# Kernel optimization log

Hardware: AMD Instinct MI355X
Metric: run time of the kernel (lower is better)

## Reference

```python
import jax, jax.numpy as jnp
import numpy as np

BATCH, INPUTDIM, OUTDIM, GRIDSIZE = 4096, 256, 256, 64


def setup_inputs() -> dict:
    key = jax.random.key(0)
    k1, k2 = jax.random.split(key)
    x = jax.random.normal(k1, (BATCH, INPUTDIM), dtype=jnp.float32)
    # xavier_uniform over (2, outdim, inputdim, gridsize): fan_in = inputdim*gridsize, fan_out = outdim*gridsize
    fan_in = INPUTDIM * GRIDSIZE
    fan_out = OUTDIM * GRIDSIZE
    limit = float(np.sqrt(6.0 / (fan_in + fan_out)))
    fouriercoeffs = jax.random.uniform(
        k2, (2, OUTDIM, INPUTDIM, GRIDSIZE), dtype=jnp.float32,
        minval=-limit, maxval=limit)
    bias = jnp.zeros((1, OUTDIM), dtype=jnp.float32)
    return {"x": x, "fouriercoeffs": fouriercoeffs, "bias": bias}


def reference(x, fouriercoeffs, bias):
    # x: [B, inputdim]; fouriercoeffs: [2, outdim, inputdim, gridsize]; bias: [1, outdim]
    # gridsize_param is clamp/round'ed to an int in torch -> static = initial_gridsize here.
    G = fouriercoeffs.shape[-1]
    k = jnp.arange(1, G + 1, dtype=x.dtype)        # [G] frequencies 1..G
    xk = x[:, :, None] * k                          # [B, inputdim, G]
    c = jnp.cos(xk)                                 # [B, inputdim, G]
    s = jnp.sin(xk)                                 # [B, inputdim, G]
    # Fused contraction over (inputdim, gridsize) -- avoids the naive
    # [B, outdim, inputdim, gridsize] broadcast tensor of the torch code.
    y = (jnp.einsum('big,oig->bo', c, fouriercoeffs[0])
         + jnp.einsum('big,oig->bo', s, fouriercoeffs[1])
         + bias)                                    # [B, outdim]
    return y
```

## Files before the change

kernel.cpp:

```cpp
#include <hip/hip_runtime.h>
#include <hip/hip_bf16.h>


typedef __attribute__((ext_vector_type(8))) short short8;
typedef __attribute__((ext_vector_type(4))) float f32x4;

#define SPLITK 8
#define ICHUNK (256 / SPLITK)

#define INV2PI 0.15915494309189535f

#if __has_builtin(__builtin_amdgcn_cvt_pk_bf16_f32)
typedef __attribute__((ext_vector_type(2))) __bf16 bf16x2_t;
__device__ __forceinline__ unsigned pkbf16(float a, float b) {
    bf16x2_t v = __builtin_amdgcn_cvt_pk_bf16_f32(a, b);
    return __builtin_bit_cast(unsigned, v);
}
#else
__device__ __forceinline__ unsigned pkbf16(float a, float b) {
    unsigned ua = __builtin_bit_cast(unsigned, a) + 0x8000u;
    unsigned ub = __builtin_bit_cast(unsigned, b) + 0x8000u;
    return __builtin_amdgcn_perm(ub, ua, 0x07060302u);
}
#endif

__device__ __forceinline__ void dbl2(float c, float s, float& co, float& so) {
    float t = c + c;
    co = __builtin_fmaf(t, c, -1.f);
    so = t * s;
}
__device__ __forceinline__ void rot2(float c, float s, float cr, float sr,
                                     float& co, float& so) {
    float t = s * sr;
    co = __builtin_fmaf(c, cr, -t);
    float u = s * cr;
    so = __builtin_fmaf(c, sr, u);
}

__device__ __forceinline__ short8 chain8(float m1, float fm1, float f0) {
    unsigned r[4];
    float vp = fm1, v = f0;
    #pragma unroll
    for (int h = 0; h < 4; ++h) {
        float v1 = __builtin_fmaf(m1, v, -vp);
        r[h] = pkbf16(v, v1);
        float v2 = __builtin_fmaf(m1, v1, -v);
        vp = v1; v = v2;
    }
    uint4 u; u.x = r[0]; u.y = r[1]; u.z = r[2]; u.w = r[3];
    return __builtin_bit_cast(short8, u);
}

__device__ __forceinline__ void async_load16(const void* g, void* l) {
    __builtin_amdgcn_global_load_lds(
        (const __attribute__((address_space(1))) unsigned int*)g,
        (__attribute__((address_space(3))) unsigned int*)l,
        16, 0, 0);
}

__global__ __launch_bounds__(256) void prep_kernel(
    const float* __restrict__ fc, const float* __restrict__ bias,
    unsigned short* __restrict__ ws2, float* __restrict__ out)
{
    const unsigned bid = blockIdx.x;
    const unsigned t = threadIdx.x;
    if (bid < 4096) {
        unsigned flat = bid * 256 + t;
        unsigned bx = flat >> 11, gi = flat & 2047;
        unsigned i = bx >> 1, y = bx & 1;
        unsigned sog = gi >> 6, ll = gi & 63;
        unsigned s = sog >> 3, og = sog & 7;
        unsigned op = og * 16 + (ll & 15);
        unsigned k = s * 32 + ((ll >> 4) * 8);
        unsigned tt = k >> 6, g0 = k & 63;
        const float4* src = (const float4*)(fc +
            ((((size_t)tt * 256 + y * 128 + op) * 256 + i) * 64 + g0));
        float4 a = src[0], b = src[1];
        uint4 v;
        v.x = pkbf16(a.x, a.y); v.y = pkbf16(a.z, a.w);
        v.z = pkbf16(b.x, b.y); v.w = pkbf16(b.z, b.w);
        ((uint4*)ws2)[flat] = v;
    } else {
        int tid = (bid - 4096) * 256 + t;
        float4 b4 = ((const float4*)bias)[tid & 63];
        ((float4*)out)[tid] = b4;
    }
}

template <bool USE_WS>
__global__ __launch_bounds__(256, 2) void fkan_gemm(
    const float* __restrict__ x, const float* __restrict__ fc,
    const unsigned short* __restrict__ bws, float* __restrict__ out)
{
    __shared__ uint4 Bimg[2][2048];
    __shared__ float xs[ICHUNK][128];

    const int t  = threadIdx.x;
    const int l  = t & 63;
    const int w  = t >> 6;
    const int wr = w >> 1, wc = w & 1;
    const int q  = l >> 4;
    const int m  = l & 15;

    const int bid = blockIdx.x;
    const int z   = bid & 7;
    const int by  = (bid >> 3) & 1;
    const int bx  = bid >> 4;
    const int rowBase = bx * 128;
    const int iBase   = z * ICHUNK;

    f32x4 acc[4][4];
    #pragma unroll
    for (int a = 0; a < 4; ++a)
        #pragma unroll
        for (int b = 0; b < 4; ++b) acc[a][b] = (f32x4)0.0f;

    auto stageB = [&](int p, int i) {
        if (USE_WS) {
            const unsigned short* base = bws + ((size_t)(i * 2 + by) * 2048) * 8;
            #pragma unroll
            for (int cc = 0; cc < 8; ++cc) {
                int c = cc * 4 + w;
                async_load16(base + (size_t)(c * 64 + l) * 8, (void*)(&Bimg[p][c * 64]));
            }
        } else {
            #pragma unroll
            for (int gg = 0; gg < 8; ++gg) {
                int gi  = gg * 256 + t;
                int sog = gi >> 6, ll = gi & 63;
                int s = sog >> 3, ogb = sog & 7;
                int o = ogb * 16 + (ll & 15);
                int k = s * 32 + (ll >> 4) * 8;
                int tt = k >> 6, g = k & 63;
                const float4* p4 = (const float4*)(fc +
                    ((((size_t)tt * 256 + by * 128 + o) * 256 + i) * 64 + g));
                float4 a = p4[0], b = p4[1];
                uint4 v;
                v.x = pkbf16(a.x, a.y); v.y = pkbf16(a.z, a.w);
                v.z = pkbf16(b.x, b.y); v.w = pkbf16(b.z, b.w);
                Bimg[p][gi] = v;
            }
        }
    };

    stageB(0, iBase);
    {
        int r = t >> 1, c0 = (t & 1) * 16;
        const float4* px = (const float4*)(x + (size_t)(rowBase + r) * 256 + iBase + c0);
        float4 v0 = px[0], v1 = px[1], v2 = px[2], v3 = px[3];
        float tmp[16] = { v0.x, v0.y, v0.z, v0.w, v1.x, v1.y, v1.z, v1.w,
                          v2.x, v2.y, v2.z, v2.w, v3.x, v3.y, v3.z, v3.w };
        #pragma unroll
        for (int j = 0; j < 16; ++j) xs[c0 + j][r] = tmp[j];
    }
    __syncthreads();

    #pragma unroll 1
    for (int ii = 0; ii < ICHUNK; ++ii) {
        const int p = ii & 1;

        if (ii + 1 < ICHUNK) stageB(p ^ 1, iBase + ii + 1);

        short8 bF[4][4];
        #pragma unroll
        for (int s = 0; s < 4; ++s)
            #pragma unroll
            for (int cf = 0; cf < 4; ++cf)
                bF[s][cf] = __builtin_bit_cast(short8,
                    Bimg[p][(s * 8 + wc * 4 + cf) * 64 + l]);

        short8 aF[4][4];
        #pragma unroll
        for (int rf = 0; rf < 4; ++rf) {
            float xv = xs[ii][wr * 64 + rf * 16 + m];
            float rev = xv * INV2PI;
            float s1 = __builtin_amdgcn_sinf(rev);
            float c1 = __builtin_amdgcn_cosf(rev);
            const float m1 = c1 + c1;
            float c2, s2, c4, s4, c8, s8, c16, s16, c32, s32;
            dbl2(c1, s1, c2, s2);
            dbl2(c2, s2, c4, s4);
            dbl2(c4, s4, c8, s8);
            dbl2(c8, s8, c16, s16);
            dbl2(c16, s16, c32, s32);
            float c24, s24;
            rot2(c16, s16, c8, s8, c24, s24);
            float cq = (q == 0) ? 1.f : (q == 1) ? c8 : (q == 2) ? c16 : c24;
            float sq = (q == 0) ? 0.f : (q == 1) ? s8 : (q == 2) ? s16 : s24;
            float cq1, sq1, cB, sB, cB1, sB1;
            rot2(cq, sq, c1, s1, cq1, sq1);
            rot2(cq, sq, c32, s32, cB, sB);
            rot2(cB, sB, c1, s1, cB1, sB1);
            aF[rf][0] = chain8(m1, cq, cq1);
            aF[rf][1] = chain8(m1, cB, cB1);
            aF[rf][2] = chain8(m1, sq, sq1);
            aF[rf][3] = chain8(m1, sB, sB1);
        }

        #pragma unroll
        for (int s = 0; s < 4; ++s)
            #pragma unroll
            for (int rf = 0; rf < 4; ++rf)
                #pragma unroll
                for (int cf = 0; cf < 4; ++cf)
                    acc[rf][cf] = __builtin_amdgcn_mfma_f32_16x16x32_bf16(
                        aF[rf][s], bF[s][cf], acc[rf][cf], 0, 0, 0);

        __syncthreads();
    }

    const int r0 = rowBase + wr * 64 + (l >> 4) * 4;
    const int c0 = by * 128 + wc * 64 + m;
    #pragma unroll
    for (int rf = 0; rf < 4; ++rf)
        #pragma unroll
        for (int cf = 0; cf < 4; ++cf)
            #pragma unroll
            for (int e = 0; e < 4; ++e)
                atomicAdd(out + (size_t)(r0 + rf * 16 + e) * 256 + (c0 + cf * 16),
                          acc[rf][cf][e]);
}

extern "C" void kernel_launch(void* const* d_in, const int* in_sizes, int n_in,
                              void* d_out, int out_size, void* d_ws, size_t ws_size,
                              hipStream_t stream) {
    const float* x    = (const float*)d_in[0];
    const float* fc   = (const float*)d_in[1];
    const float* bias = (const float*)d_in[2];
    float* out = (float*)d_out;
    unsigned short* bws = (unsigned short*)d_ws;

    const size_t wsNeed = (size_t)512 * 2048 * 16;
    hipLaunchKernelGGL(prep_kernel, dim3(5120), dim3(256), 0, stream,
                       fc, bias, bws, out);
    if (ws_size >= wsNeed) {
        hipLaunchKernelGGL((fkan_gemm<true>), dim3(512), dim3(256), 0, stream,
                           x, fc, bws, out);
    } else {
        hipLaunchKernelGGL((fkan_gemm<false>), dim3(512), dim3(256), 0, stream,
                           x, fc, bws, out);
    }
}
```

Before: 177.1 us.

## Replace split-K atomic adds with partial buffers and a separate reduce kernel

Each split-K block now writes its partial tile to a per-slice workspace buffer with plain stores. A new reduce kernel then sums the eight slices and adds the bias. This removes contended global float atomics on the output, but adds a third launch and about 32 MB of extra partial-buffer writes and reads. The old atomic path is kept as a fallback when the workspace is too small.

```diff
diff --git a/kernel.cpp b/kernel.cpp
--- a/kernel.cpp
+++ b/kernel.cpp
@@ -60,9 +60,9 @@
 
 __global__ __launch_bounds__(256) void prep_kernel(
     const float* __restrict__ fc, const float* __restrict__ bias,
-    unsigned short* __restrict__ ws2, float* __restrict__ out)
+    unsigned short* __restrict__ ws2, float* __restrict__ out, int base)
 {
-    const unsigned bid = blockIdx.x;
+    const unsigned bid = blockIdx.x + base;
     const unsigned t = threadIdx.x;
     if (bid < 4096) {
         unsigned flat = bid * 256 + t;
@@ -87,10 +87,26 @@
     }
 }
 
-template <bool USE_WS>
+__global__ __launch_bounds__(256) void reduce_kernel(
+    const float* __restrict__ pws, const float* __restrict__ bias,
+    float* __restrict__ out)
+{
+    int idx4 = blockIdx.x * 256 + threadIdx.x;
+    const float4* p4 = (const float4*)pws;
+    float4 r = ((const float4*)bias)[idx4 & 63];
+    #pragma unroll
+    for (int z = 0; z < SPLITK; ++z) {
+        float4 v = p4[(size_t)z * 262144 + idx4];
+        r.x += v.x; r.y += v.y; r.z += v.z; r.w += v.w;
+    }
+    ((float4*)out)[idx4] = r;
+}
+
+template <bool USE_WS, bool PARTIAL>
 __global__ __launch_bounds__(256, 2) void fkan_gemm(
     const float* __restrict__ x, const float* __restrict__ fc,
-    const unsigned short* __restrict__ bws, float* __restrict__ out)
+    const unsigned short* __restrict__ bws, float* __restrict__ out,
+    float* __restrict__ pws)
 {
     __shared__ uint4 Bimg[2][2048];
     __shared__ float xs[ICHUNK][128];
@@ -211,14 +227,26 @@
 
     const int r0 = rowBase + wr * 64 + (l >> 4) * 4;
     const int c0 = by * 128 + wc * 64 + m;
-    #pragma unroll
-    for (int rf = 0; rf < 4; ++rf)
-        #pragma unroll
-        for (int cf = 0; cf < 4; ++cf)
-            #pragma unroll
-            for (int e = 0; e < 4; ++e)
-                atomicAdd(out + (size_t)(r0 + rf * 16 + e) * 256 + (c0 + cf * 16),
-                          acc[rf][cf][e]);
+    if (PARTIAL) {
+        float* dst = pws + (size_t)z * (4096 * 256);
+        #pragma unroll
+        for (int rf = 0; rf < 4; ++rf)
+            #pragma unroll
+            for (int cf = 0; cf < 4; ++cf)
+                #pragma unroll
+                for (int e = 0; e < 4; ++e)
+                    dst[(size_t)(r0 + rf * 16 + e) * 256 + (c0 + cf * 16)] =
+                        acc[rf][cf][e];
+    } else {
+        #pragma unroll
+        for (int rf = 0; rf < 4; ++rf)
+            #pragma unroll
+            for (int cf = 0; cf < 4; ++cf)
+                #pragma unroll
+                for (int e = 0; e < 4; ++e)
+                    atomicAdd(out + (size_t)(r0 + rf * 16 + e) * 256 + (c0 + cf * 16),
+                              acc[rf][cf][e]);
+    }
 }
 
 extern "C" void kernel_launch(void* const* d_in, const int* in_sizes, int n_in,
@@ -230,14 +258,26 @@
     float* out = (float*)d_out;
     unsigned short* bws = (unsigned short*)d_ws;
 
-    const size_t wsNeed = (size_t)512 * 2048 * 16;
-    hipLaunchKernelGGL(prep_kernel, dim3(5120), dim3(256), 0, stream,
-                       fc, bias, bws, out);
-    if (ws_size >= wsNeed) {
-        hipLaunchKernelGGL((fkan_gemm<true>), dim3(512), dim3(256), 0, stream,
-                           x, fc, bws, out);
+    const size_t wsCoeff = (size_t)512 * 2048 * 16;
+    const size_t wsFull  = wsCoeff + (size_t)SPLITK * 4096 * 256 * 4;
+    float* pws = (float*)((char*)d_ws + wsCoeff);
+
+    if (ws_size >= wsFull) {
+        hipLaunchKernelGGL(prep_kernel, dim3(4096), dim3(256), 0, stream,
+                           fc, bias, bws, out, 0);
+        hipLaunchKernelGGL((fkan_gemm<true, true>), dim3(512), dim3(256), 0, stream,
+                           x, fc, bws, out, pws);
+        hipLaunchKernelGGL(reduce_kernel, dim3(1024), dim3(256), 0, stream,
+                           pws, bias, out);
+    } else if (ws_size >= wsCoeff) {
+        hipLaunchKernelGGL(prep_kernel, dim3(5120), dim3(256), 0, stream,
+                           fc, bias, bws, out, 0);
+        hipLaunchKernelGGL((fkan_gemm<true, false>), dim3(512), dim3(256), 0, stream,
+                           x, fc, bws, out, pws);
     } else {
-        hipLaunchKernelGGL((fkan_gemm<false>), dim3(512), dim3(256), 0, stream,
-                           x, fc, bws, out);
-    }
-}
+        hipLaunchKernelGGL(prep_kernel, dim3(1024), dim3(256), 0, stream,
+                           fc, bias, bws, out, 4096);
+        hipLaunchKernelGGL((fkan_gemm<false, false>), dim3(512), dim3(256), 0, stream,
+                           x, fc, bws, out, pws);
+    }
+}
```

Measured after the change: 173.6 us. 1.02x faster.
